# Kernel tuning notes

Hardware: AMD Instinct MI355X
Metric: run time of the kernel (lower is better)

## Reference

```python
import jax, jax.numpy as jnp
import numpy as np

EPS = 1e-8
PAD = 1  # kernel // 2 for kernel=3


def setup_inputs() -> dict:
    key = jax.random.key(0)
    k1, k2, k3, k4, k5 = jax.random.split(key, 5)
    b, c, h, w = 16, 256, 64, 64
    out_ch, kernel, style_dim = 256, 3, 512
    x = jax.random.normal(k1, (b, c, h, w), dtype=jnp.float32)
    style = jax.random.normal(k2, (b, style_dim), dtype=jnp.float32)
    # learned params
    weight = jax.random.normal(k3, (1, out_ch, c, kernel, kernel), dtype=jnp.float32)
    lim = 1.0 / np.sqrt(style_dim)
    mod_w = jax.random.uniform(k4, (c, style_dim), minval=-lim, maxval=lim, dtype=jnp.float32)
    mod_b = jax.random.uniform(k5, (c,), minval=-lim, maxval=lim, dtype=jnp.float32)
    return {"x": x, "style": style, "weight": weight, "mod_w": mod_w, "mod_b": mod_b}


def reference(x, style, weight, mod_w, mod_b):
    # s[b,i]: per-sample, per-input-channel modulation from the style Linear
    s = style @ mod_w.T + mod_b                     # [b, in_ch]
    w = weight[0]                                    # [out_ch, in_ch, k, k]
    # demod factor: sum_{i,kh,kw} (w[o,i,kh,kw]*s[b,i])^2 = sum_i s^2 * sum_kk w^2
    w_sq = jnp.sum(w * w, axis=(2, 3))               # [out_ch, in_ch]
    d = jax.lax.rsqrt(jnp.einsum('oi,bi->bo', w_sq, s * s) + EPS)  # [b, out_ch]
    # modulate input channels instead of materializing per-sample weights
    xs = x * s[:, :, None, None]                     # [b, in_ch, h, w]
    y = jax.lax.conv_general_dilated(
        xs, w, window_strides=(1, 1), padding=[(PAD, PAD), (PAD, PAD)],
        dimension_numbers=('NCHW', 'OIHW', 'NCHW'))
    return y * d[:, :, None, None]                   # [b, out_ch, h, w]
```

## Files before the change

### kernel.cpp

```cpp
#include <hip/hip_runtime.h>
#include <hip/hip_bf16.h>
#include <cstdint>
#include <cstddef>

typedef __bf16 bf16_t;
typedef __bf16 bf16x4 __attribute__((ext_vector_type(4)));
typedef __bf16 bf16x8 __attribute__((ext_vector_type(8)));
typedef float  f32x4  __attribute__((ext_vector_type(4)));

#define NB   16
#define NC   256
#define NO   256
#define SD   512
#define NPIX 4096
#define CPAD 36

#define WS_S   0
#define WS_D   16384
#define WS_WSQ 32768
#define WS_WT  294912

__global__ __launch_bounds__(256) void prep1(
    const float* __restrict__ style, const float* __restrict__ weight,
    const float* __restrict__ mod_w, const float* __restrict__ mod_b,
    float* __restrict__ s_buf, float* __restrict__ wsq, bf16_t* __restrict__ wT)
{
    const int blk = blockIdx.x;
    const int tid = threadIdx.x;
    if (blk < 16) {
        const int b = blk, i = tid;
        const float* st = style + b * SD;
        const float* mw = mod_w + i * SD;
        float acc = 0.f;
        for (int k = 0; k < SD; k += 4) {
            float4 a = *(const float4*)(st + k);
            float4 c = *(const float4*)(mw + k);
            acc += a.x * c.x + a.y * c.y + a.z * c.z + a.w * c.w;
        }
        s_buf[b * NC + i] = acc + mod_b[i];
    } else {
        const int o = blk - 16, i = tid;
        const float* wp = weight + (o * NC + i) * 9;
        float q = 0.f;
        #pragma unroll
        for (int t = 0; t < 9; ++t) {
            float v = wp[t];
            q += v * v;
            wT[t * (NO * NC) + o * NC + i] = (bf16_t)v;
        }
        wsq[o * NC + i] = q;
    }
}

__global__ __launch_bounds__(256) void prep2(
    const float* __restrict__ s_buf, const float* __restrict__ wsq,
    float* __restrict__ d_buf)
{
    const int b = blockIdx.x, o = threadIdx.x;
    const float* wq = wsq + o * NC;
    const float* sb = s_buf + b * NC;
    float sum = 0.f;
    for (int i = 0; i < NC; ++i) {
        float sv = sb[i];
        sum += wq[i] * sv * sv;
    }
    d_buf[b * NC + o] = rsqrtf(sum + 1e-8f);
}

__device__ __forceinline__ void stage_a(const bf16_t* __restrict__ wT_tap,
                                        int o0, int ic0, bf16_t* dst, int tid)
{
    #pragma unroll
    for (int it = 0; it < 2; ++it) {
        int s = it * 256 + tid;
        const bf16_t* g = wT_tap + (o0 + (s >> 2)) * NC + ic0 + (s & 3) * 8;
        __builtin_amdgcn_global_load_lds(
            (const __attribute__((address_space(1))) void*)g,
            (__attribute__((address_space(3))) void*)(dst + s * 8),
            16, 0, 0);
    }
}

__global__ __launch_bounds__(256) void conv_mfma(
    const float* __restrict__ x,
    const bf16_t* __restrict__ wT,
    const float* __restrict__ s_buf,
    const float* __restrict__ d_buf,
    float* __restrict__ out)
{
    __shared__ bf16_t lds_a[2][128 * 32];
    __shared__ bf16_t lds_b[4 * 64 * CPAD];

    const int tid   = threadIdx.x;
    const int lane  = tid & 63;
    const int wv    = tid >> 6;
    const int wo    = wv >> 1;
    const int wp    = wv & 1;
    const int pt    = blockIdx.x;
    const int o0    = blockIdx.y * 128;
    const int batch = blockIdx.z;
    const int row0  = pt * 2;

    const int l15 = lane & 15;
    const int k0  = (lane >> 4) * 8;

    const int colB = tid & 63;
    const int cgrp = tid >> 6;

    f32x4 acc[4][4];
    #pragma unroll
    for (int i = 0; i < 4; ++i)
        #pragma unroll
        for (int j = 0; j < 4; ++j) {
            f32x4 z = {0.f, 0.f, 0.f, 0.f};
            acc[i][j] = z;
        }

    bf16x8 bzero;
    #pragma unroll
    for (int j = 0; j < 8; ++j) bzero[j] = (bf16_t)0.f;

    for (int chunk = 0; chunk < 8; ++chunk) {
        const int ic0 = chunk * 32;

        {
            float sv[8];
            #pragma unroll
            for (int c = 0; c < 8; ++c)
                sv[c] = s_buf[batch * NC + ic0 + cgrp * 8 + c];
            const float* xbase = x + (size_t)(batch * NC + ic0 + cgrp * 8) * NPIX + colB;
            #pragma unroll
            for (int r = 0; r < 4; ++r) {
                const int gy = row0 - 1 + r;
                const bool valid = ((unsigned)gy < 64u);
                const int lbase = (r * 64 + colB) * CPAD + cgrp * 8;
                #pragma unroll
                for (int cp = 0; cp < 4; ++cp) {
                    float v0 = 0.f, v1 = 0.f;
                    if (valid) {
                        v0 = xbase[(2 * cp)     * NPIX + gy * 64] * sv[2 * cp];
                        v1 = xbase[(2 * cp + 1) * NPIX + gy * 64] * sv[2 * cp + 1];
                    }
                    union { bf16_t h[2]; uint32_t u; } pk;
                    pk.h[0] = (bf16_t)v0;
                    pk.h[1] = (bf16_t)v1;
                    *(uint32_t*)&lds_b[lbase + 2 * cp] = pk.u;
                }
            }
        }
        stage_a(wT, o0, ic0, &lds_a[0][0], tid);
        __syncthreads();

        #pragma unroll
        for (int tap = 0; tap < 9; ++tap) {
            if (tap < 8)
                stage_a(wT + (tap + 1) * (NO * NC), o0, ic0,
                        &lds_a[(tap + 1) & 1][0], tid);

            const bf16_t* abuf = &lds_a[tap & 1][0];
            const int kh = tap / 3, kw = tap % 3;

            bf16x8 af[4];
            #pragma unroll
            for (int of = 0; of < 4; ++of)
                af[of] = *(const bf16x8*)&abuf[(wo * 64 + of * 16 + l15) * 32 + k0];

            const int r = wp + kh;
            bf16x8 bfr[4];
            #pragma unroll
            for (int nf = 0; nf < 4; ++nf) {
                const int c = nf * 16 + l15 + kw - 1;
                if ((unsigned)c < 64u) {
                    const bf16_t* p = &lds_b[(r * 64 + c) * CPAD + k0];
                    bf16x4 lo = *(const bf16x4*)p;
                    bf16x4 hi = *(const bf16x4*)(p + 4);
                    bfr[nf] = __builtin_shufflevector(lo, hi, 0, 1, 2, 3, 4, 5, 6, 7);
                } else {
                    bfr[nf] = bzero;
                }
            }

            #pragma unroll
            for (int of = 0; of < 4; ++of)
                #pragma unroll
                for (int nf = 0; nf < 4; ++nf)
                    acc[of][nf] = __builtin_amdgcn_mfma_f32_16x16x32_bf16(
                        af[of], bfr[nf], acc[of][nf], 0, 0, 0);

            __syncthreads();
        }
    }

    const int p_base = pt * 128 + wp * 64;
    #pragma unroll
    for (int of = 0; of < 4; ++of) {
        #pragma unroll
        for (int rg = 0; rg < 4; ++rg) {
            const int o_g = o0 + wo * 64 + of * 16 + (lane >> 4) * 4 + rg;
            const float dv = d_buf[batch * NO + o_g];
            const size_t obase = (size_t)(batch * NO + o_g) * NPIX;
            #pragma unroll
            for (int nf = 0; nf < 4; ++nf) {
                const int p_g = p_base + nf * 16 + l15;
                out[obase + p_g] = acc[of][nf][rg] * dv;
            }
        }
    }
}

extern "C" void kernel_launch(void* const* d_in, const int* in_sizes, int n_in,
                              void* d_out, int out_size, void* d_ws, size_t ws_size,
                              hipStream_t stream)
{
    const float* x      = (const float*)d_in[0];
    const float* style  = (const float*)d_in[1];
    const float* weight = (const float*)d_in[2];
    const float* mod_w  = (const float*)d_in[3];
    const float* mod_b  = (const float*)d_in[4];
    float* out = (float*)d_out;

    char* ws = (char*)d_ws;
    float*  s_buf = (float*)(ws + WS_S);
    float*  d_buf = (float*)(ws + WS_D);
    float*  wsq   = (float*)(ws + WS_WSQ);
    bf16_t* wT    = (bf16_t*)(ws + WS_WT);

    hipLaunchKernelGGL(prep1, dim3(272), dim3(256), 0, stream,
                       style, weight, mod_w, mod_b, s_buf, wsq, wT);
    hipLaunchKernelGGL(prep2, dim3(16), dim3(256), 0, stream, s_buf, wsq, d_buf);
    hipLaunchKernelGGL(conv_mfma, dim3(32, 2, 16), dim3(256), 0, stream,
                       x, wT, s_buf, d_buf, out);
}
```

Before: 260.3 us.

## Load weight fragments directly to registers and double-buffer input tile in LDS

Weight A-fragments are now loaded straight from global memory into registers and prefetched one tap ahead, replacing the LDS staging of weights. The modulated input tile is double-buffered in LDS, so the next channel chunk is staged while MFMAs run on the current one. This drops the per-tap block barrier to one barrier per chunk, and launch bounds now ask for 3 waves per SIMD. The trade-off is that each wave reads weights from global or L2 with no LDS sharing across waves, and register pressure rises from the prefetch buffers.

```diff
diff --git a/kernel.cpp b/kernel.cpp
--- a/kernel.cpp
+++ b/kernel.cpp
@@ -67,29 +67,14 @@
     d_buf[b * NC + o] = rsqrtf(sum + 1e-8f);
 }
 
-__device__ __forceinline__ void stage_a(const bf16_t* __restrict__ wT_tap,
-                                        int o0, int ic0, bf16_t* dst, int tid)
-{
-    #pragma unroll
-    for (int it = 0; it < 2; ++it) {
-        int s = it * 256 + tid;
-        const bf16_t* g = wT_tap + (o0 + (s >> 2)) * NC + ic0 + (s & 3) * 8;
-        __builtin_amdgcn_global_load_lds(
-            (const __attribute__((address_space(1))) void*)g,
-            (__attribute__((address_space(3))) void*)(dst + s * 8),
-            16, 0, 0);
-    }
-}
-
-__global__ __launch_bounds__(256) void conv_mfma(
+__global__ __launch_bounds__(256, 3) void conv_mfma(
     const float* __restrict__ x,
     const bf16_t* __restrict__ wT,
     const float* __restrict__ s_buf,
     const float* __restrict__ d_buf,
     float* __restrict__ out)
 {
-    __shared__ bf16_t lds_a[2][128 * 32];
-    __shared__ bf16_t lds_b[4 * 64 * CPAD];
+    __shared__ bf16_t lds_b[2][4 * 64 * CPAD];
 
     const int tid   = threadIdx.x;
     const int lane  = tid & 63;
@@ -120,50 +105,66 @@
     #pragma unroll
     for (int j = 0; j < 8; ++j) bzero[j] = (bf16_t)0.f;
 
+    auto STAGE = [&](int ic0, bf16_t* __restrict__ dst) {
+        const float* sp = s_buf + batch * NC + ic0 + cgrp * 8;
+        float4 sa = *(const float4*)sp;
+        float4 sb = *(const float4*)(sp + 4);
+        float sv[8] = {sa.x, sa.y, sa.z, sa.w, sb.x, sb.y, sb.z, sb.w};
+        const float* xbase = x + (size_t)(batch * NC + ic0 + cgrp * 8) * NPIX + colB;
+        float v[4][8];
+        #pragma unroll
+        for (int r = 0; r < 4; ++r) {
+            const int gy = row0 - 1 + r;
+            const bool valid = ((unsigned)gy < 64u);
+            const float* rp = xbase + gy * 64;
+            #pragma unroll
+            for (int j = 0; j < 8; ++j)
+                v[r][j] = valid ? rp[j * NPIX] : 0.f;
+        }
+        #pragma unroll
+        for (int r = 0; r < 4; ++r) {
+            const int lbase = (r * 64 + colB) * CPAD + cgrp * 8;
+            #pragma unroll
+            for (int half = 0; half < 2; ++half) {
+                union { bf16_t h[4]; uint2 u; } pk;
+                #pragma unroll
+                for (int j = 0; j < 4; ++j)
+                    pk.h[j] = (bf16_t)(v[r][half * 4 + j] * sv[half * 4 + j]);
+                *(uint2*)&dst[lbase + half * 4] = pk.u;
+            }
+        }
+    };
+
+    const size_t TSTR = (size_t)NO * NC;
+    const bf16_t* aBase = wT + (size_t)(o0 + wo * 64 + l15) * NC + k0;
+
+    bf16x8 af[4];
+    #pragma unroll
+    for (int of = 0; of < 4; ++of)
+        af[of] = *(const bf16x8*)(aBase + of * 16 * NC);
+    STAGE(0, &lds_b[0][0]);
+    __syncthreads();
+
     for (int chunk = 0; chunk < 8; ++chunk) {
         const int ic0 = chunk * 32;
-
-        {
-            float sv[8];
-            #pragma unroll
-            for (int c = 0; c < 8; ++c)
-                sv[c] = s_buf[batch * NC + ic0 + cgrp * 8 + c];
-            const float* xbase = x + (size_t)(batch * NC + ic0 + cgrp * 8) * NPIX + colB;
-            #pragma unroll
-            for (int r = 0; r < 4; ++r) {
-                const int gy = row0 - 1 + r;
-                const bool valid = ((unsigned)gy < 64u);
-                const int lbase = (r * 64 + colB) * CPAD + cgrp * 8;
-                #pragma unroll
-                for (int cp = 0; cp < 4; ++cp) {
-                    float v0 = 0.f, v1 = 0.f;
-                    if (valid) {
-                        v0 = xbase[(2 * cp)     * NPIX + gy * 64] * sv[2 * cp];
-                        v1 = xbase[(2 * cp + 1) * NPIX + gy * 64] * sv[2 * cp + 1];
-                    }
-                    union { bf16_t h[2]; uint32_t u; } pk;
-                    pk.h[0] = (bf16_t)v0;
-                    pk.h[1] = (bf16_t)v1;
-                    *(uint32_t*)&lds_b[lbase + 2 * cp] = pk.u;
-                }
-            }
-        }
-        stage_a(wT, o0, ic0, &lds_a[0][0], tid);
-        __syncthreads();
-
-        #pragma unroll
+        if (chunk < 7)
+            STAGE(ic0 + 32, &lds_b[(chunk + 1) & 1][0]);
+
+        const bf16_t* bbuf = &lds_b[chunk & 1][0];
+        const bf16_t* aChunk = aBase + ic0;
+        const bf16_t* aNextChunk = aBase + (chunk < 7 ? ic0 + 32 : ic0);
+
+        #pragma unroll 1
         for (int tap = 0; tap < 9; ++tap) {
-            if (tap < 8)
-                stage_a(wT + (tap + 1) * (NO * NC), o0, ic0,
-                        &lds_a[(tap + 1) & 1][0], tid);
-
-            const bf16_t* abuf = &lds_a[tap & 1][0];
-            const int kh = tap / 3, kw = tap % 3;
-
-            bf16x8 af[4];
+            const int kh = tap / 3;
+            const int kw = tap - kh * 3;
+
+            const bf16_t* aN = (tap < 8) ? (aChunk + (size_t)(tap + 1) * TSTR)
+                                         : aNextChunk;
+            bf16x8 afn[4];
             #pragma unroll
             for (int of = 0; of < 4; ++of)
-                af[of] = *(const bf16x8*)&abuf[(wo * 64 + of * 16 + l15) * 32 + k0];
+                afn[of] = *(const bf16x8*)(aN + of * 16 * NC);
 
             const int r = wp + kh;
             bf16x8 bfr[4];
@@ -171,7 +172,7 @@
             for (int nf = 0; nf < 4; ++nf) {
                 const int c = nf * 16 + l15 + kw - 1;
                 if ((unsigned)c < 64u) {
-                    const bf16_t* p = &lds_b[(r * 64 + c) * CPAD + k0];
+                    const bf16_t* p = &bbuf[(r * 64 + c) * CPAD + k0];
                     bf16x4 lo = *(const bf16x4*)p;
                     bf16x4 hi = *(const bf16x4*)(p + 4);
                     bfr[nf] = __builtin_shufflevector(lo, hi, 0, 1, 2, 3, 4, 5, 6, 7);
@@ -187,8 +188,10 @@
                     acc[of][nf] = __builtin_amdgcn_mfma_f32_16x16x32_bf16(
                         af[of], bfr[nf], acc[of][nf], 0, 0, 0);
 
-            __syncthreads();
-        }
+            #pragma unroll
+            for (int of = 0; of < 4; ++of) af[of] = afn[of];
+        }
+        __syncthreads();
     }
 
     const int p_base = pt * 128 + wp * 64;
```

Result: slower. 302.5 us (+16.2%).

## Re-layout LDS tiles for 16-byte conflict-free reads and vectorize input staging

Applied to the files above, without the earlier changes.

Changes the weight-tile LDS layout to be k-group-major, so each lane's 8-element A fragment is a contiguous 16-byte read with fewer bank conflicts. It also changes the B tile padding from 36 to 40, which allows single 128-bit B fragment loads instead of two 64-bit loads. Input staging now loads s as float4 and writes 8 channels per thread as one uint4 LDS store, batching global loads across two rows. Adds a launch bound of three blocks per CU, which may force register spilling given the 64-float accumulator.

```diff
diff --git a/kernel.cpp b/kernel.cpp
--- a/kernel.cpp
+++ b/kernel.cpp
@@ -13,7 +13,7 @@
 #define NO   256
 #define SD   512
 #define NPIX 4096
-#define CPAD 36
+#define CPAD 40
 
 #define WS_S   0
 #define WS_D   16384
@@ -73,7 +73,7 @@
     #pragma unroll
     for (int it = 0; it < 2; ++it) {
         int s = it * 256 + tid;
-        const bf16_t* g = wT_tap + (o0 + (s >> 2)) * NC + ic0 + (s & 3) * 8;
+        const bf16_t* g = wT_tap + (o0 + (s & 127)) * NC + ic0 + (s >> 7) * 8;
         __builtin_amdgcn_global_load_lds(
             (const __attribute__((address_space(1))) void*)g,
             (__attribute__((address_space(3))) void*)(dst + s * 8),
@@ -81,14 +81,14 @@
     }
 }
 
-__global__ __launch_bounds__(256) void conv_mfma(
+__global__ __launch_bounds__(256, 3) void conv_mfma(
     const float* __restrict__ x,
     const bf16_t* __restrict__ wT,
     const float* __restrict__ s_buf,
     const float* __restrict__ d_buf,
     float* __restrict__ out)
 {
-    __shared__ bf16_t lds_a[2][128 * 32];
+    __shared__ bf16_t lds_a[2][4096];
     __shared__ bf16_t lds_b[4 * 64 * CPAD];
 
     const int tid   = threadIdx.x;
@@ -102,7 +102,8 @@
     const int row0  = pt * 2;
 
     const int l15 = lane & 15;
-    const int k0  = (lane >> 4) * 8;
+    const int kg  = lane >> 4;
+    const int k0  = kg * 8;
 
     const int colB = tid & 63;
     const int cgrp = tid >> 6;
@@ -120,41 +121,50 @@
     #pragma unroll
     for (int j = 0; j < 8; ++j) bzero[j] = (bf16_t)0.f;
 
+    auto STAGE = [&](int ic0) {
+        const float* sp = s_buf + batch * NC + ic0 + cgrp * 8;
+        float4 sa = *(const float4*)sp;
+        float4 sb = *(const float4*)(sp + 4);
+        float sv[8] = {sa.x, sa.y, sa.z, sa.w, sb.x, sb.y, sb.z, sb.w};
+        const float* xbase = x + (size_t)(batch * NC + ic0 + cgrp * 8) * NPIX + colB;
+        #pragma unroll
+        for (int rh = 0; rh < 2; ++rh) {
+            float v[2][8];
+            #pragma unroll
+            for (int rr = 0; rr < 2; ++rr) {
+                const int r = rh * 2 + rr;
+                const int gy = row0 - 1 + r;
+                const bool valid = ((unsigned)gy < 64u);
+                const float* rp = xbase + gy * 64;
+                #pragma unroll
+                for (int j = 0; j < 8; ++j)
+                    v[rr][j] = valid ? rp[j * NPIX] : 0.f;
+            }
+            #pragma unroll
+            for (int rr = 0; rr < 2; ++rr) {
+                const int r = rh * 2 + rr;
+                union { bf16_t h[8]; uint4 u; } pk;
+                #pragma unroll
+                for (int j = 0; j < 8; ++j)
+                    pk.h[j] = (bf16_t)(v[rr][j] * sv[j]);
+                *(uint4*)&lds_b[(r * 64 + colB) * CPAD + cgrp * 8] = pk.u;
+            }
+        }
+    };
+
+    const size_t TSTR = (size_t)NO * NC;
+
     for (int chunk = 0; chunk < 8; ++chunk) {
         const int ic0 = chunk * 32;
 
-        {
-            float sv[8];
-            #pragma unroll
-            for (int c = 0; c < 8; ++c)
-                sv[c] = s_buf[batch * NC + ic0 + cgrp * 8 + c];
-            const float* xbase = x + (size_t)(batch * NC + ic0 + cgrp * 8) * NPIX + colB;
-            #pragma unroll
-            for (int r = 0; r < 4; ++r) {
-                const int gy = row0 - 1 + r;
-                const bool valid = ((unsigned)gy < 64u);
-                const int lbase = (r * 64 + colB) * CPAD + cgrp * 8;
-                #pragma unroll
-                for (int cp = 0; cp < 4; ++cp) {
-                    float v0 = 0.f, v1 = 0.f;
-                    if (valid) {
-                        v0 = xbase[(2 * cp)     * NPIX + gy * 64] * sv[2 * cp];
-                        v1 = xbase[(2 * cp + 1) * NPIX + gy * 64] * sv[2 * cp + 1];
-                    }
-                    union { bf16_t h[2]; uint32_t u; } pk;
-                    pk.h[0] = (bf16_t)v0;
-                    pk.h[1] = (bf16_t)v1;
-                    *(uint32_t*)&lds_b[lbase + 2 * cp] = pk.u;
-                }
-            }
-        }
+        STAGE(ic0);
         stage_a(wT, o0, ic0, &lds_a[0][0], tid);
         __syncthreads();
 
         #pragma unroll
         for (int tap = 0; tap < 9; ++tap) {
             if (tap < 8)
-                stage_a(wT + (tap + 1) * (NO * NC), o0, ic0,
+                stage_a(wT + (size_t)(tap + 1) * TSTR, o0, ic0,
                         &lds_a[(tap + 1) & 1][0], tid);
 
             const bf16_t* abuf = &lds_a[tap & 1][0];
@@ -163,7 +173,7 @@
             bf16x8 af[4];
             #pragma unroll
             for (int of = 0; of < 4; ++of)
-                af[of] = *(const bf16x8*)&abuf[(wo * 64 + of * 16 + l15) * 32 + k0];
+                af[of] = *(const bf16x8*)&abuf[kg * 1024 + (wo * 64 + of * 16 + l15) * 8];
 
             const int r = wp + kh;
             bf16x8 bfr[4];
@@ -171,10 +181,7 @@
             for (int nf = 0; nf < 4; ++nf) {
                 const int c = nf * 16 + l15 + kw - 1;
                 if ((unsigned)c < 64u) {
-                    const bf16_t* p = &lds_b[(r * 64 + c) * CPAD + k0];
-                    bf16x4 lo = *(const bf16x4*)p;
-                    bf16x4 hi = *(const bf16x4*)(p + 4);
-                    bfr[nf] = __builtin_shufflevector(lo, hi, 0, 1, 2, 3, 4, 5, 6, 7);
+                    bfr[nf] = *(const bf16x8*)&lds_b[(r * 64 + c) * CPAD + k0];
                 } else {
                     bfr[nf] = bzero;
                 }
```

Result: slower. 278.2 us (+6.9%).
